# Kernel tuning notes

Measured on AMD Instinct MI355X. Metric: run time of the kernel, lower is better.

The kernel has to match this reference:

```python
import jax, jax.numpy as jnp
import numpy as np

N = 50000      # nodes
E = 800000     # edges (avg degree 16)
G = 256        # graphs in batch
IN = 128       # in_channels
H = 256        # hidden_channels
L = 4          # num_layers


def setup_inputs() -> dict:
    key = jax.random.key(0)
    ks = jax.random.split(key, 16)
    x = jax.random.normal(ks[0], (N, IN), dtype=jnp.float32)
    edge_index = jax.random.randint(ks[1], (2, E), 0, N, dtype=jnp.int64)
    batch = jnp.sort(jax.random.randint(ks[2], (N,), 0, G, dtype=jnp.int64))
    s_in = 1.0 / np.sqrt(IN)
    s_h = 1.0 / np.sqrt(H)
    return {
        "x": x,
        "edge_index": edge_index,
        "batch": batch,
        "w1_0": jax.random.normal(ks[3], (IN, H), jnp.float32) * s_in,
        "b1_0": jnp.zeros((H,), jnp.float32),
        "w2_0": jax.random.normal(ks[4], (H, H), jnp.float32) * s_h,
        "b2_0": jnp.zeros((H,), jnp.float32),
        "w1s": jax.random.normal(ks[5], (L - 1, H, H), jnp.float32) * s_h,
        "b1s": jnp.zeros((L - 1, H), jnp.float32),
        "w2s": jax.random.normal(ks[6], (L - 1, H, H), jnp.float32) * s_h,
        "b2s": jnp.zeros((L - 1, H), jnp.float32),
    }


def reference(x, edge_index, batch, w1_0, b1_0, w2_0, b2_0, w1s, b1s, w2s, b2s):
    n_nodes = x.shape[0]
    src, dst = edge_index[0], edge_index[1]

    def gin_layer(h, w1, b1, w2, b2):
        # scatter-add neighbor aggregation: out[i] = sum_{(j->i)} h[j]
        agg = jax.ops.segment_sum(h[src], dst, num_segments=n_nodes)
        z = h + agg  # GIN with eps = 0: (1+eps)*x + aggr
        z = jax.nn.relu(z @ w1 + b1) @ w2 + b2  # MLP: Linear-ReLU-Linear
        return jax.nn.relu(z)  # outer F.relu in forward

    h = gin_layer(x, w1_0, b1_0, w2_0, b2_0)
    for i in range(L - 1):  # small fixed layer loop
        h = gin_layer(h, w1s[i], b1s[i], w2s[i], b2s[i])

    # global_add_pool: per-graph segment sum -> [G, H]
    return jax.ops.segment_sum(h, batch, num_segments=G)
```

## Files before the change

kernel.cpp:

```cpp
#include <hip/hip_runtime.h>
#include <hip/hip_bf16.h>

#define NN 50000
#define NE 800000
#define NG 256
#define CIN 128
#define CH 256
#define CAP 64

typedef unsigned short u16;
typedef unsigned int u32;
typedef unsigned char u8;
typedef __attribute__((ext_vector_type(8))) short short8;
typedef __attribute__((ext_vector_type(8))) unsigned short ushort8;
typedef __attribute__((ext_vector_type(4))) float f32x4;

__device__ __forceinline__ float bf2f(u16 u) { return __uint_as_float(((u32)u) << 16); }
__device__ __forceinline__ u16 f2bf(float f) {
    u32 u = __float_as_uint(f);
    return (u16)((u + 0x7fffu + ((u >> 16) & 1u)) >> 16);
}

__global__ void k_prep(const float* __restrict__ x, u16* __restrict__ xb,
                       const float* __restrict__ w1_0, const float* __restrict__ w2_0,
                       const float* __restrict__ w1s, const float* __restrict__ w2s,
                       u16* __restrict__ Wp, int* __restrict__ deg,
                       float* __restrict__ outf,
                       float* __restrict__ S0, float* __restrict__ S1) {
    int t = blockIdx.x * 256 + threadIdx.x;
    if (t < NN) deg[t] = 0;
    if (t < NG * CH) outf[t] = 0.f;
    if (t < CIN) xb[(size_t)NN * CIN + t] = 0;
    if (t == 0) { S0[NN] = 0.f; S1[NN] = 0.f; }
    if (t < NN * CIN / 4) {
        float4 v = ((const float4*)x)[t];
        ushort4 o; o.x = f2bf(v.x); o.y = f2bf(v.y); o.z = f2bf(v.z); o.w = f2bf(v.w);
        ((ushort4*)xb)[t] = o;
    }
    if (t < CIN * CH + 7 * CH * CH) {
        const float* Wsrc; int rem;
        if (t < CIN * CH) { Wsrc = w1_0; rem = t; }
        else {
            int o = t - CIN * CH;
            int m = o >> 16; rem = o & 65535;
            Wsrc = (m == 0) ? w2_0
                 : (m <= 3) ? w1s + (size_t)(m - 1) * 65536
                            : w2s + (size_t)(m - 4) * 65536;
        }
        int j = rem & 7, lane = (rem >> 3) & 63, nt = (rem >> 9) & 15, kb = rem >> 13;
        int k = kb * 32 + ((lane >> 4) << 3) + j;
        int nc = nt * 16 + (lane & 15);
        Wp[t] = f2bf(Wsrc[k * CH + nc]);
    }
}

__global__ void k_build(const int* __restrict__ dst, const int* __restrict__ src,
                        int* __restrict__ deg, int* __restrict__ col) {
    int e = blockIdx.x * 256 + threadIdx.x;
    if (e < NE) {
        int d = dst[e];
        int pos = atomicAdd(&deg[d], 1);
        col[d * CAP + pos] = src[e];
    }
}

#define ZS 264
template <int K1, bool QIN, bool QOUT, bool POOL>
__global__ __launch_bounds__(256, 6) void k_layer(const u16* __restrict__ G,
                                                  const int* __restrict__ deg,
                                                  const int* __restrict__ col,
                                                  const u8* __restrict__ Qin,
                                                  const float* __restrict__ Sin,
                                                  const u16* __restrict__ Wp1,
                                                  const float* __restrict__ b1,
                                                  const u16* __restrict__ Wp2,
                                                  const float* __restrict__ b2,
                                                  u16* __restrict__ out,
                                                  u8* __restrict__ Qout,
                                                  float* __restrict__ Sout,
                                                  const int* __restrict__ batchp,
                                                  float* __restrict__ outf) {
    __shared__ __align__(16) u16 zs[32 * ZS];
    const int tid = threadIdx.x;
    const int wave = tid >> 6, lane = tid & 63;
    const int quad = lane >> 4, l16 = lane & 15;
    const int m0 = blockIdx.x * 32;

    if (!QIN) {
        constexpr int LPR = K1 / 8;
        constexpr int RPG = 64 / LPR;
        const int sub = lane / LPR;
        const int c0 = (lane % LPR) * 8;
        for (int g = 0; g < 8; g += RPG) {
            int lr = wave * 8 + g + sub;
            int r = m0 + lr; if (r >= NN) r = NN - 1;
            const u16* base = G + c0;
            float a[8];
            ushort8 sv = *(const ushort8*)(base + (size_t)r * K1);
#pragma unroll
            for (int i = 0; i < 8; i++) a[i] = bf2f(sv[i]);
            int beg = r * CAP, end = beg + deg[r];
            for (int e = beg; e < end; e += 8) {
                int4 ca = *(const int4*)(col + e);
                int4 cb = *(const int4*)(col + e + 4);
                int idx[8] = {ca.x, ca.y, ca.z, ca.w, cb.x, cb.y, cb.z, cb.w};
#pragma unroll
                for (int u = 0; u < 8; u++)
                    if (e + u >= end) idx[u] = NN;
                ushort8 v[8];
#pragma unroll
                for (int u = 0; u < 8; u++)
                    v[u] = *(const ushort8*)(base + (size_t)idx[u] * K1);
#pragma unroll
                for (int u = 0; u < 8; u++)
#pragma unroll
                    for (int i = 0; i < 8; i++) a[i] += bf2f(v[u][i]);
            }
            ushort8 o;
#pragma unroll
            for (int i = 0; i < 8; i++) o[i] = f2bf(a[i]);
            *(ushort8*)(zs + lr * ZS + c0) = o;
        }
    } else {
        const int sub = lane >> 4;
        const int c0 = (lane & 15) * 16;
        for (int g = 0; g < 8; g += 4) {
            int lr = wave * 8 + g + sub;
            int r = m0 + lr; if (r >= NN) r = NN - 1;
            float a[16];
            const u16* sp = G + (size_t)r * CH + c0;
            ushort8 s0v = *(const ushort8*)sp;
            ushort8 s1v = *(const ushort8*)(sp + 8);
#pragma unroll
            for (int i = 0; i < 8; i++) { a[i] = bf2f(s0v[i]); a[8 + i] = bf2f(s1v[i]); }
            int beg = r * CAP, end = beg + deg[r];
            for (int e = beg; e < end; e += 4) {
                int4 ca = *(const int4*)(col + e);
                int idx[4] = {ca.x, ca.y, ca.z, ca.w};
#pragma unroll
                for (int u = 0; u < 4; u++)
                    if (e + u >= end) idx[u] = NN;
                uint4 qv[4]; float sc[4];
#pragma unroll
                for (int u = 0; u < 4; u++) {
                    qv[u] = *(const uint4*)(Qin + (size_t)idx[u] * CH + c0);
                    sc[u] = Sin[idx[u]];
                }
#pragma unroll
                for (int u = 0; u < 4; u++) {
#pragma unroll
                    for (int d = 0; d < 4; d++) {
                        u32 w = ((const u32*)&qv[u])[d];
                        a[d * 4 + 0] += sc[u] * (float)(w & 0xffu);
                        a[d * 4 + 1] += sc[u] * (float)((w >> 8) & 0xffu);
                        a[d * 4 + 2] += sc[u] * (float)((w >> 16) & 0xffu);
                        a[d * 4 + 3] += sc[u] * (float)(w >> 24);
                    }
                }
            }
            ushort8 o0, o1;
#pragma unroll
            for (int i = 0; i < 8; i++) { o0[i] = f2bf(a[i]); o1[i] = f2bf(a[8 + i]); }
            *(ushort8*)(zs + lr * ZS + c0) = o0;
            *(ushort8*)(zs + lr * ZS + c0 + 8) = o1;
        }
    }
    __syncthreads();

    f32x4 acc[2][4];
#pragma unroll
    for (int ri = 0; ri < 2; ri++)
#pragma unroll
        for (int nj = 0; nj < 4; nj++) acc[ri][nj] = (f32x4){0.f, 0.f, 0.f, 0.f};

    const u16* w1b = Wp1 + (wave * 4) * 512 + lane * 8;
    const u16* w2b = Wp2 + (wave * 4) * 512 + lane * 8;
    constexpr int KB1 = K1 / 32;
    short8 b_cur[4], b_nxt[4];
#pragma unroll
    for (int nj = 0; nj < 4; nj++) b_cur[nj] = *(const short8*)(w1b + nj * 512);

#pragma unroll
    for (int kb = 0; kb < KB1; kb++) {
        int kn = (kb + 1 < KB1) ? (kb + 1) : kb;
#pragma unroll
        for (int nj = 0; nj < 4; nj++)
            b_nxt[nj] = *(const short8*)(w1b + kn * 8192 + nj * 512);
        short8 a[2];
#pragma unroll
        for (int ri = 0; ri < 2; ri++)
            a[ri] = *(const short8*)(zs + (ri * 16 + l16) * ZS + kb * 32 + quad * 8);
#pragma unroll
        for (int nj = 0; nj < 4; nj++)
#pragma unroll
            for (int ri = 0; ri < 2; ri++)
                acc[ri][nj] = __builtin_amdgcn_mfma_f32_16x16x32_bf16(a[ri], b_cur[nj], acc[ri][nj], 0, 0, 0);
#pragma unroll
        for (int nj = 0; nj < 4; nj++) b_cur[nj] = b_nxt[nj];
    }

    short8 b2_cur[4];
#pragma unroll
    for (int nj = 0; nj < 4; nj++) b2_cur[nj] = *(const short8*)(w2b + nj * 512);

    __syncthreads();

#pragma unroll
    for (int nj = 0; nj < 4; nj++) {
        int cc = wave * 64 + nj * 16 + l16;
        float bv = b1[cc];
#pragma unroll
        for (int ri = 0; ri < 2; ri++) {
            f32x4 v = acc[ri][nj];
#pragma unroll
            for (int j = 0; j < 4; j++)
                zs[(ri * 16 + quad * 4 + j) * ZS + cc] = f2bf(fmaxf(v[j] + bv, 0.f));
        }
    }
    __syncthreads();

#pragma unroll
    for (int ri = 0; ri < 2; ri++)
#pragma unroll
        for (int nj = 0; nj < 4; nj++) acc[ri][nj] = (f32x4){0.f, 0.f, 0.f, 0.f};

#pragma unroll
    for (int kb = 0; kb < 8; kb++) {
        int kn = (kb + 1 < 8) ? (kb + 1) : kb;
#pragma unroll
        for (int nj = 0; nj < 4; nj++)
            b_nxt[nj] = *(const short8*)(w2b + kn * 8192 + nj * 512);
        short8 a[2];
#pragma unroll
        for (int ri = 0; ri < 2; ri++)
            a[ri] = *(const short8*)(zs + (ri * 16 + l16) * ZS + kb * 32 + quad * 8);
#pragma unroll
        for (int nj = 0; nj < 4; nj++)
#pragma unroll
            for (int ri = 0; ri < 2; ri++)
                acc[ri][nj] = __builtin_amdgcn_mfma_f32_16x16x32_bf16(a[ri], b2_cur[nj], acc[ri][nj], 0, 0, 0);
#pragma unroll
        for (int nj = 0; nj < 4; nj++) b2_cur[nj] = b_nxt[nj];
    }
    __syncthreads();

#pragma unroll
    for (int nj = 0; nj < 4; nj++) {
        int cc = wave * 64 + nj * 16 + l16;
        float bv = b2[cc];
#pragma unroll
        for (int ri = 0; ri < 2; ri++) {
            f32x4 v = acc[ri][nj];
#pragma unroll
            for (int j = 0; j < 4; j++)
                zs[(ri * 16 + quad * 4 + j) * ZS + cc] = f2bf(fmaxf(v[j] + bv, 0.f));
        }
    }
    __syncthreads();

    if (!POOL) {
        int row = tid >> 3, cb = (tid & 7) * 32;
        int r = m0 + row;
        if (r < NN) {
            uint4* dst = (uint4*)(out + (size_t)r * CH + cb);
            const u16* srcp = zs + row * ZS + cb;
#pragma unroll
            for (int c = 0; c < 4; c++) dst[c] = *(const uint4*)(srcp + c * 8);
            if (QOUT) {
                float vloc[32]; float mx = 0.f;
#pragma unroll
                for (int c = 0; c < 32; c++) { vloc[c] = bf2f(srcp[c]); mx = fmaxf(mx, vloc[c]); }
                mx = fmaxf(mx, __shfl_xor(mx, 1));
                mx = fmaxf(mx, __shfl_xor(mx, 2));
                mx = fmaxf(mx, __shfl_xor(mx, 4));
                float inv = mx > 0.f ? 255.f / mx : 0.f;
                u32 qw[8];
#pragma unroll
                for (int d = 0; d < 8; d++) {
                    u32 q0 = (u32)(vloc[d * 4 + 0] * inv + 0.5f);
                    u32 q1 = (u32)(vloc[d * 4 + 1] * inv + 0.5f);
                    u32 q2 = (u32)(vloc[d * 4 + 2] * inv + 0.5f);
                    u32 q3 = (u32)(vloc[d * 4 + 3] * inv + 0.5f);
                    qw[d] = q0 | (q1 << 8) | (q2 << 16) | (q3 << 24);
                }
                uint4* qdst = (uint4*)(Qout + (size_t)r * CH + cb);
                qdst[0] = *(const uint4*)&qw[0];
                qdst[1] = *(const uint4*)&qw[4];
                if ((tid & 7) == 0) Sout[r] = mx * (1.f / 255.f);
            }
        }
    } else {
        int c = tid;
        float acc2 = 0.f;
        int cur_g = batchp[m0];
        for (int row = 0; row < 32; row++) {
            int r = m0 + row;
            if (r >= NN) break;
            int g = batchp[r];
            if (g != cur_g) {
                atomicAdd(&outf[cur_g * CH + c], acc2);
                acc2 = 0.f; cur_g = g;
            }
            acc2 += bf2f(zs[row * ZS + c]);
        }
        atomicAdd(&outf[cur_g * CH + c], acc2);
    }
}

extern "C" void kernel_launch(void* const* d_in, const int* in_sizes, int n_in,
                              void* d_out, int out_size, void* d_ws, size_t ws_size,
                              hipStream_t stream) {
    const float* x     = (const float*)d_in[0];
    const int*   ei    = (const int*)d_in[1];
    const int*   batch = (const int*)d_in[2];
    const float* w1_0  = (const float*)d_in[3];
    const float* b1_0  = (const float*)d_in[4];
    const float* w2_0  = (const float*)d_in[5];
    const float* b2_0  = (const float*)d_in[6];
    const float* w1s   = (const float*)d_in[7];
    const float* b1s   = (const float*)d_in[8];
    const float* w2s   = (const float*)d_in[9];
    const float* b2s   = (const float*)d_in[10];
    float* out = (float*)d_out;

    char* p = (char*)d_ws;
    u16* Hb  = (u16*)p; p += (size_t)(NN + 1) * CH * 2;
    u16* Tb  = (u16*)p; p += (size_t)(NN + 1) * CH * 2;
    u16* xb  = (u16*)p; p += (size_t)(NN + 1) * CIN * 2;
    u16* WpA = (u16*)p; p += (size_t)(CIN * CH + 7 * CH * CH) * 2;
    int* deg = (int*)p; p += (size_t)NN * 4;
    int* col = (int*)p; p += (size_t)NN * CAP * 4;
    u8*  Q0  = (u8*)p;  p += (size_t)(NN + 1) * CH;
    u8*  Q1  = (u8*)p;  p += (size_t)(NN + 1) * CH;
    float* S0 = (float*)p; p += (size_t)(NN + 1) * 4;
    float* S1 = (float*)p; p += (size_t)(NN + 1) * 4;

    u16* Wp1_0 = WpA;
    u16* Wp2_0 = Wp1_0 + CIN * CH;
    u16* Wp1sA = Wp2_0 + CH * CH;
    u16* Wp2sA = Wp1sA + 3 * CH * CH;

    const int* srcv = ei;
    const int* dstv = ei + NE;

    hipLaunchKernelGGL(k_prep, dim3((NN * CIN / 4 + 255) / 256), dim3(256), 0, stream,
                       x, xb, w1_0, w2_0, w1s, w2s, WpA, deg, out, S0, S1);

    hipLaunchKernelGGL(k_build, dim3((NE + 255) / 256), dim3(256), 0, stream,
                       dstv, srcv, deg, col);

    int layerBlocks = (NN + 31) / 32;

    hipLaunchKernelGGL((k_layer<128, false, true, false>), dim3(layerBlocks), dim3(256), 0, stream,
                       xb, deg, col, (const u8*)nullptr, (const float*)nullptr,
                       Wp1_0, b1_0, Wp2_0, b2_0, Hb, Q0, S0, batch, out);
    hipLaunchKernelGGL((k_layer<256, true, true, false>), dim3(layerBlocks), dim3(256), 0, stream,
                       Hb, deg, col, Q0, S0,
                       Wp1sA, b1s, Wp2sA, b2s, Tb, Q1, S1, batch, out);
    hipLaunchKernelGGL((k_layer<256, true, true, false>), dim3(layerBlocks), dim3(256), 0, stream,
                       Tb, deg, col, Q1, S1,
                       Wp1sA + (size_t)CH * CH, b1s + CH,
                       Wp2sA + (size_t)CH * CH, b2s + CH, Hb, Q0, S0, batch, out);
    hipLaunchKernelGGL((k_layer<256, true, false, true>), dim3(layerBlocks), dim3(256), 0, stream,
                       Hb, deg, col, Q0, S0,
                       Wp1sA + (size_t)2 * CH * CH, b1s + 2 * CH,
                       Wp2sA + (size_t)2 * CH * CH, b2s + 2 * CH,
                       (u16*)nullptr, (u8*)nullptr, (float*)nullptr, batch, out);
}
```

Before: 400.9 us.

## Split neighbor gather into separate wave-per-row kernels and compress column indices to u16

The neighbor aggregation is moved out of the fused layer kernel into dedicated gather kernels that assign one wavefront per node. Neighbor indices are made wave-uniform with readfirstlane, and each lane reads a small contiguous slice of the feature row. Column indices are stored as 16-bit values and the build kernel processes four edges per thread. The layer kernel now just loads the precomputed aggregate into shared memory before the MLP. This aims at better gather coalescing and occupancy, at the cost of extra launches and a round trip of the aggregate through global memory. Because every layer now writes in place to single Hb/Qb/Sb buffers, the k_gather_q reading Hb/Qb/Sb and the k_layer writing them are serialized on one stream, so this stays correct.

```diff
diff --git a/kernel.cpp b/kernel.cpp
--- a/kernel.cpp
+++ b/kernel.cpp
@@ -25,13 +25,12 @@
                        const float* __restrict__ w1_0, const float* __restrict__ w2_0,
                        const float* __restrict__ w1s, const float* __restrict__ w2s,
                        u16* __restrict__ Wp, int* __restrict__ deg,
-                       float* __restrict__ outf,
-                       float* __restrict__ S0, float* __restrict__ S1) {
+                       float* __restrict__ outf, float* __restrict__ S) {
     int t = blockIdx.x * 256 + threadIdx.x;
     if (t < NN) deg[t] = 0;
     if (t < NG * CH) outf[t] = 0.f;
     if (t < CIN) xb[(size_t)NN * CIN + t] = 0;
-    if (t == 0) { S0[NN] = 0.f; S1[NN] = 0.f; }
+    if (t == 0) S[NN] = 0.f;
     if (t < NN * CIN / 4) {
         float4 v = ((const float4*)x)[t];
         ushort4 o; o.x = f2bf(v.x); o.y = f2bf(v.y); o.z = f2bf(v.z); o.w = f2bf(v.w);
@@ -55,22 +54,96 @@
 }
 
 __global__ void k_build(const int* __restrict__ dst, const int* __restrict__ src,
-                        int* __restrict__ deg, int* __restrict__ col) {
-    int e = blockIdx.x * 256 + threadIdx.x;
-    if (e < NE) {
-        int d = dst[e];
-        int pos = atomicAdd(&deg[d], 1);
-        col[d * CAP + pos] = src[e];
-    }
+                        int* __restrict__ deg, u16* __restrict__ colu) {
+    int t = blockIdx.x * 256 + threadIdx.x;
+    if (t < NE / 4) {
+        int4 d4 = ((const int4*)dst)[t];
+        int4 s4 = ((const int4*)src)[t];
+        int dd[4] = {d4.x, d4.y, d4.z, d4.w};
+        int ss[4] = {s4.x, s4.y, s4.z, s4.w};
+#pragma unroll
+        for (int u = 0; u < 4; u++) {
+            int pos = atomicAdd(&deg[dd[u]], 1);
+            colu[dd[u] * CAP + pos] = (u16)ss[u];
+        }
+    }
+}
+
+__global__ __launch_bounds__(256, 8) void k_gather_x(const u16* __restrict__ xb,
+                                                     const int* __restrict__ deg,
+                                                     const u16* __restrict__ colu,
+                                                     u16* __restrict__ Z) {
+    const int lane = threadIdx.x & 63;
+    const int r = __builtin_amdgcn_readfirstlane(blockIdx.x * 4 + (threadIdx.x >> 6));
+    const int co = lane * 2;
+    u32 sv = *(const u32*)(xb + (size_t)r * CIN + co);
+    float a0 = __uint_as_float(sv << 16);
+    float a1 = __uint_as_float(sv & 0xffff0000u);
+    const int dg = deg[r];
+    const u16* cb = colu + r * CAP;
+    for (int e = 0; e < dg; e += 8) {
+        ushort8 cv = *(const ushort8*)(cb + e);
+        int idx[8];
+#pragma unroll
+        for (int u = 0; u < 8; u++) {
+            int id = (e + u < dg) ? (int)cv[u] : NN;
+            idx[u] = __builtin_amdgcn_readfirstlane(id);
+        }
+        u32 qw[8];
+#pragma unroll
+        for (int u = 0; u < 8; u++)
+            qw[u] = *(const u32*)(xb + (size_t)idx[u] * CIN + co);
+#pragma unroll
+        for (int u = 0; u < 8; u++) {
+            a0 += __uint_as_float(qw[u] << 16);
+            a1 += __uint_as_float(qw[u] & 0xffff0000u);
+        }
+    }
+    u32 o = (u32)f2bf(a0) | ((u32)f2bf(a1) << 16);
+    *(u32*)(Z + (size_t)r * CIN + co) = o;
+}
+
+__global__ __launch_bounds__(256, 8) void k_gather_q(const u16* __restrict__ G,
+                                                     const u8* __restrict__ Qin,
+                                                     const float* __restrict__ Sin,
+                                                     const int* __restrict__ deg,
+                                                     const u16* __restrict__ colu,
+                                                     u16* __restrict__ Z) {
+    const int lane = threadIdx.x & 63;
+    const int r = __builtin_amdgcn_readfirstlane(blockIdx.x * 4 + (threadIdx.x >> 6));
+    const int co = lane * 4;
+    ushort4 sv = *(const ushort4*)(G + (size_t)r * CH + co);
+    float a0 = bf2f(sv.x), a1 = bf2f(sv.y), a2 = bf2f(sv.z), a3 = bf2f(sv.w);
+    const int dg = deg[r];
+    const u16* cb = colu + r * CAP;
+    for (int e = 0; e < dg; e += 8) {
+        ushort8 cv = *(const ushort8*)(cb + e);
+        int idx[8]; float sc[8];
+#pragma unroll
+        for (int u = 0; u < 8; u++) {
+            int id = (e + u < dg) ? (int)cv[u] : NN;
+            idx[u] = __builtin_amdgcn_readfirstlane(id);
+            sc[u] = Sin[idx[u]];
+        }
+        u32 qw[8];
+#pragma unroll
+        for (int u = 0; u < 8; u++)
+            qw[u] = *(const u32*)(Qin + (size_t)idx[u] * CH + co);
+#pragma unroll
+        for (int u = 0; u < 8; u++) {
+            a0 += sc[u] * (float)(qw[u] & 0xffu);
+            a1 += sc[u] * (float)((qw[u] >> 8) & 0xffu);
+            a2 += sc[u] * (float)((qw[u] >> 16) & 0xffu);
+            a3 += sc[u] * (float)(qw[u] >> 24);
+        }
+    }
+    ushort4 o; o.x = f2bf(a0); o.y = f2bf(a1); o.z = f2bf(a2); o.w = f2bf(a3);
+    *(ushort4*)(Z + (size_t)r * CH + co) = o;
 }
 
 #define ZS 264
-template <int K1, bool QIN, bool QOUT, bool POOL>
-__global__ __launch_bounds__(256, 6) void k_layer(const u16* __restrict__ G,
-                                                  const int* __restrict__ deg,
-                                                  const int* __restrict__ col,
-                                                  const u8* __restrict__ Qin,
-                                                  const float* __restrict__ Sin,
+template <int K1, bool QOUT, bool POOL>
+__global__ __launch_bounds__(256, 6) void k_layer(const u16* __restrict__ Z,
                                                   const u16* __restrict__ Wp1,
                                                   const float* __restrict__ b1,
                                                   const u16* __restrict__ Wp2,
@@ -86,84 +159,14 @@
     const int quad = lane >> 4, l16 = lane & 15;
     const int m0 = blockIdx.x * 32;
 
-    if (!QIN) {
-        constexpr int LPR = K1 / 8;
-        constexpr int RPG = 64 / LPR;
-        const int sub = lane / LPR;
-        const int c0 = (lane % LPR) * 8;
-        for (int g = 0; g < 8; g += RPG) {
-            int lr = wave * 8 + g + sub;
-            int r = m0 + lr; if (r >= NN) r = NN - 1;
-            const u16* base = G + c0;
-            float a[8];
-            ushort8 sv = *(const ushort8*)(base + (size_t)r * K1);
-#pragma unroll
-            for (int i = 0; i < 8; i++) a[i] = bf2f(sv[i]);
-            int beg = r * CAP, end = beg + deg[r];
-            for (int e = beg; e < end; e += 8) {
-                int4 ca = *(const int4*)(col + e);
-                int4 cb = *(const int4*)(col + e + 4);
-                int idx[8] = {ca.x, ca.y, ca.z, ca.w, cb.x, cb.y, cb.z, cb.w};
-#pragma unroll
-                for (int u = 0; u < 8; u++)
-                    if (e + u >= end) idx[u] = NN;
-                ushort8 v[8];
-#pragma unroll
-                for (int u = 0; u < 8; u++)
-                    v[u] = *(const ushort8*)(base + (size_t)idx[u] * K1);
-#pragma unroll
-                for (int u = 0; u < 8; u++)
-#pragma unroll
-                    for (int i = 0; i < 8; i++) a[i] += bf2f(v[u][i]);
-            }
-            ushort8 o;
-#pragma unroll
-            for (int i = 0; i < 8; i++) o[i] = f2bf(a[i]);
-            *(ushort8*)(zs + lr * ZS + c0) = o;
-        }
-    } else {
-        const int sub = lane >> 4;
-        const int c0 = (lane & 15) * 16;
-        for (int g = 0; g < 8; g += 4) {
-            int lr = wave * 8 + g + sub;
-            int r = m0 + lr; if (r >= NN) r = NN - 1;
-            float a[16];
-            const u16* sp = G + (size_t)r * CH + c0;
-            ushort8 s0v = *(const ushort8*)sp;
-            ushort8 s1v = *(const ushort8*)(sp + 8);
-#pragma unroll
-            for (int i = 0; i < 8; i++) { a[i] = bf2f(s0v[i]); a[8 + i] = bf2f(s1v[i]); }
-            int beg = r * CAP, end = beg + deg[r];
-            for (int e = beg; e < end; e += 4) {
-                int4 ca = *(const int4*)(col + e);
-                int idx[4] = {ca.x, ca.y, ca.z, ca.w};
-#pragma unroll
-                for (int u = 0; u < 4; u++)
-                    if (e + u >= end) idx[u] = NN;
-                uint4 qv[4]; float sc[4];
-#pragma unroll
-                for (int u = 0; u < 4; u++) {
-                    qv[u] = *(const uint4*)(Qin + (size_t)idx[u] * CH + c0);
-                    sc[u] = Sin[idx[u]];
-                }
-#pragma unroll
-                for (int u = 0; u < 4; u++) {
-#pragma unroll
-                    for (int d = 0; d < 4; d++) {
-                        u32 w = ((const u32*)&qv[u])[d];
-                        a[d * 4 + 0] += sc[u] * (float)(w & 0xffu);
-                        a[d * 4 + 1] += sc[u] * (float)((w >> 8) & 0xffu);
-                        a[d * 4 + 2] += sc[u] * (float)((w >> 16) & 0xffu);
-                        a[d * 4 + 3] += sc[u] * (float)(w >> 24);
-                    }
-                }
-            }
-            ushort8 o0, o1;
-#pragma unroll
-            for (int i = 0; i < 8; i++) { o0[i] = f2bf(a[i]); o1[i] = f2bf(a[8 + i]); }
-            *(ushort8*)(zs + lr * ZS + c0) = o0;
-            *(ushort8*)(zs + lr * ZS + c0 + 8) = o1;
-        }
+    {
+        int row = tid >> 3, ccb = (tid & 7) * (K1 / 8);
+        int r = m0 + row; if (r >= NN) r = NN - 1;
+        const u16* zp = Z + (size_t)r * K1 + ccb;
+        u16* zd = zs + row * ZS + ccb;
+#pragma unroll
+        for (int c = 0; c < K1 / 64; c++)
+            *(ushort8*)(zd + c * 8) = *(const ushort8*)(zp + c * 8);
     }
     __syncthreads();
 
@@ -324,16 +327,14 @@
     float* out = (float*)d_out;
 
     char* p = (char*)d_ws;
-    u16* Hb  = (u16*)p; p += (size_t)(NN + 1) * CH * 2;
-    u16* Tb  = (u16*)p; p += (size_t)(NN + 1) * CH * 2;
+    u16* Hb  = (u16*)p; p += (size_t)NN * CH * 2;
+    u16* Zb  = (u16*)p; p += (size_t)NN * CH * 2;
     u16* xb  = (u16*)p; p += (size_t)(NN + 1) * CIN * 2;
     u16* WpA = (u16*)p; p += (size_t)(CIN * CH + 7 * CH * CH) * 2;
     int* deg = (int*)p; p += (size_t)NN * 4;
-    int* col = (int*)p; p += (size_t)NN * CAP * 4;
-    u8*  Q0  = (u8*)p;  p += (size_t)(NN + 1) * CH;
-    u8*  Q1  = (u8*)p;  p += (size_t)(NN + 1) * CH;
-    float* S0 = (float*)p; p += (size_t)(NN + 1) * 4;
-    float* S1 = (float*)p; p += (size_t)(NN + 1) * 4;
+    u16* colu= (u16*)p; p += (size_t)NN * CAP * 2;
+    u8*  Qb  = (u8*)p;  p += (size_t)(NN + 1) * CH;
+    float* Sb= (float*)p; p += (size_t)(NN + 1) * 4;
 
     u16* Wp1_0 = WpA;
     u16* Wp2_0 = Wp1_0 + CIN * CH;
@@ -343,27 +344,35 @@
     const int* srcv = ei;
     const int* dstv = ei + NE;
 
+    int gatherBlocks = NN / 4;
+    int layerBlocks  = (NN + 31) / 32;
+
     hipLaunchKernelGGL(k_prep, dim3((NN * CIN / 4 + 255) / 256), dim3(256), 0, stream,
-                       x, xb, w1_0, w2_0, w1s, w2s, WpA, deg, out, S0, S1);
-
-    hipLaunchKernelGGL(k_build, dim3((NE + 255) / 256), dim3(256), 0, stream,
-                       dstv, srcv, deg, col);
-
-    int layerBlocks = (NN + 31) / 32;
-
-    hipLaunchKernelGGL((k_layer<128, false, true, false>), dim3(layerBlocks), dim3(256), 0, stream,
-                       xb, deg, col, (const u8*)nullptr, (const float*)nullptr,
-                       Wp1_0, b1_0, Wp2_0, b2_0, Hb, Q0, S0, batch, out);
-    hipLaunchKernelGGL((k_layer<256, true, true, false>), dim3(layerBlocks), dim3(256), 0, stream,
-                       Hb, deg, col, Q0, S0,
-                       Wp1sA, b1s, Wp2sA, b2s, Tb, Q1, S1, batch, out);
-    hipLaunchKernelGGL((k_layer<256, true, true, false>), dim3(layerBlocks), dim3(256), 0, stream,
-                       Tb, deg, col, Q1, S1,
-                       Wp1sA + (size_t)CH * CH, b1s + CH,
-                       Wp2sA + (size_t)CH * CH, b2s + CH, Hb, Q0, S0, batch, out);
-    hipLaunchKernelGGL((k_layer<256, true, false, true>), dim3(layerBlocks), dim3(256), 0, stream,
-                       Hb, deg, col, Q0, S0,
-                       Wp1sA + (size_t)2 * CH * CH, b1s + 2 * CH,
+                       x, xb, w1_0, w2_0, w1s, w2s, WpA, deg, out, Sb);
+
+    hipLaunchKernelGGL(k_build, dim3((NE / 4 + 255) / 256), dim3(256), 0, stream,
+                       dstv, srcv, deg, colu);
+
+    hipLaunchKernelGGL(k_gather_x, dim3(gatherBlocks), dim3(256), 0, stream,
+                       xb, deg, colu, Zb);
+    hipLaunchKernelGGL((k_layer<128, true, false>), dim3(layerBlocks), dim3(256), 0, stream,
+                       Zb, Wp1_0, b1_0, Wp2_0, b2_0, Hb, Qb, Sb, batch, out);
+
+    hipLaunchKernelGGL(k_gather_q, dim3(gatherBlocks), dim3(256), 0, stream,
+                       Hb, Qb, Sb, deg, colu, Zb);
+    hipLaunchKernelGGL((k_layer<256, true, false>), dim3(layerBlocks), dim3(256), 0, stream,
+                       Zb, Wp1sA, b1s, Wp2sA, b2s, Hb, Qb, Sb, batch, out);
+
+    hipLaunchKernelGGL(k_gather_q, dim3(gatherBlocks), dim3(256), 0, stream,
+                       Hb, Qb, Sb, deg, colu, Zb);
+    hipLaunchKernelGGL((k_layer<256, true, false>), dim3(layerBlocks), dim3(256), 0, stream,
+                       Zb, Wp1sA + (size_t)CH * CH, b1s + CH,
+                       Wp2sA + (size_t)CH * CH, b2s + CH, Hb, Qb, Sb, batch, out);
+
+    hipLaunchKernelGGL(k_gather_q, dim3(gatherBlocks), dim3(256), 0, stream,
+                       Hb, Qb, Sb, deg, colu, Zb);
+    hipLaunchKernelGGL((k_layer<256, false, true>), dim3(layerBlocks), dim3(256), 0, stream,
+                       Zb, Wp1sA + (size_t)2 * CH * CH, b1s + 2 * CH,
                        Wp2sA + (size_t)2 * CH * CH, b2s + 2 * CH,
                        (u16*)nullptr, (u8*)nullptr, (float*)nullptr, batch, out);
 }
```

Result: slower. 422.9 us (+5.5%).
